# Performance work log

Measured on AMD Instinct MI355X. Metric: run time of the kernel, lower is better.

Reference implementation:

```python
import jax, jax.numpy as jnp
import numpy as np

B, CIN, T = 32, 64, 4096
E, H, HD, FF, L = 256, 8, 32, 1024, 4
K, S = 15, 2
SEQ = 512
GROUPS = E // 2
EPS = 1e-5


def setup_inputs() -> dict:
    key = jax.random.key(0)
    ks = jax.random.split(key, 16)
    d = {}
    d['x'] = jax.random.normal(ks[0], (B, CIN, T), jnp.float32)
    d['conv0_w'] = jax.random.normal(ks[1], (E, CIN, K), jnp.float32) * 0.03
    d['conv0_b'] = jnp.zeros((E,), jnp.float32)
    d['conv12_w'] = jax.random.normal(ks[2], (2, E, E, K), jnp.float32) * 0.016
    d['conv12_b'] = jnp.zeros((2, E), jnp.float32)
    d['gn_g'] = jnp.ones((3, E), jnp.float32)
    d['gn_b'] = jnp.zeros((3, E), jnp.float32)
    d['Wq'] = jax.random.normal(ks[3], (L, H, HD, E), jnp.float32) * 0.0625
    d['Wk'] = jax.random.normal(ks[4], (L, H, HD, E), jnp.float32) * 0.0625
    d['Wv'] = jax.random.normal(ks[5], (L, H, HD, E), jnp.float32) * 0.0625
    d['Wo'] = jax.random.normal(ks[6], (L, E, E), jnp.float32) * 0.0625
    d['ln1_g'] = jnp.ones((L, E), jnp.float32)
    d['ln1_b'] = jnp.zeros((L, E), jnp.float32)
    d['Wf1'] = jax.random.normal(ks[7], (L, FF, E), jnp.float32) * 0.0625
    d['bf1'] = jnp.zeros((L, FF), jnp.float32)
    d['Wf2'] = jax.random.normal(ks[8], (L, E, FF), jnp.float32) * 0.03125
    d['bf2'] = jnp.zeros((L, E), jnp.float32)
    d['ln2_g'] = jnp.ones((L, E), jnp.float32)
    d['ln2_b'] = jnp.zeros((L, E), jnp.float32)
    d['Wc1'] = jax.random.normal(ks[9], (256, SEQ * E), jnp.float32) * 0.003
    d['bc1'] = jnp.zeros((256,), jnp.float32)
    d['Wc2'] = jax.random.normal(ks[10], (1, 256), jnp.float32) * 0.0625
    d['bc2'] = jnp.zeros((1,), jnp.float32)
    return d


def conv1d(x, w, b, stride, pad):
    y = jax.lax.conv_general_dilated(x, w, (stride,), [(pad, pad)],
                                     dimension_numbers=('NCH', 'OIH', 'NCH'))
    return y + b[None, :, None]


def group_norm(x, g, b):
    # x: [B, C, Len]; torch GroupNorm with C//2 groups
    Bn, C, Ln = x.shape
    xg = x.reshape(Bn, GROUPS, C // GROUPS, Ln)
    mu = xg.mean(axis=(2, 3), keepdims=True)
    var = ((xg - mu) ** 2).mean(axis=(2, 3), keepdims=True)
    xn = ((xg - mu) * jax.lax.rsqrt(var + EPS)).reshape(Bn, C, Ln)
    return xn * g[None, :, None] + b[None, :, None]


def layer_norm(x, g, b):
    mu = x.mean(-1, keepdims=True)
    var = ((x - mu) ** 2).mean(-1, keepdims=True)
    return (x - mu) * jax.lax.rsqrt(var + EPS) * g + b


def pos_encoding(seq, e):
    t = jnp.arange(seq, dtype=jnp.float32)[:, None]
    i = jnp.arange(e, dtype=jnp.float32)[None, :]
    ang = t / jnp.power(10000.0, i / e)  # note: i/e, matching the source
    return jnp.where(jnp.arange(e)[None, :] % 2 == 0, jnp.sin(ang), jnp.cos(ang))


def reference(x, conv0_w, conv0_b, conv12_w, conv12_b, gn_g, gn_b,
              Wq, Wk, Wv, Wo, ln1_g, ln1_b, Wf1, bf1, Wf2, bf2,
              ln2_g, ln2_b, Wc1, bc1, Wc2, bc2):
    # --- conv encoder: (conv -> dropout(eval) -> groupnorm -> gelu) x3 ---
    h = conv1d(x, conv0_w, conv0_b, S, K // 2)
    h = jax.nn.gelu(group_norm(h, gn_g[0], gn_b[0]), approximate=False)
    for i in range(2):
        h = conv1d(h, conv12_w[i], conv12_b[i], S, K // 2)
        h = jax.nn.gelu(group_norm(h, gn_g[i + 1], gn_b[i + 1]), approximate=False)
    h = jnp.transpose(h, (0, 2, 1))  # [B, SEQ, E]

    # --- transformer encoder ---
    h = h + pos_encoding(h.shape[1], E)[None]
    scale = 1.0 / jnp.sqrt(jnp.float32(HD))
    for l in range(L):
        q = jnp.einsum('bse,hde->bhsd', h, Wq[l])
        k = jnp.einsum('bse,hde->bhsd', h, Wk[l])
        v = jnp.einsum('bse,hde->bhsd', h, Wv[l])
        attn = jax.nn.softmax(jnp.einsum('bhqd,bhkd->bhqk', q, k) * scale, axis=-1)
        o = jnp.einsum('bhqk,bhkd->bhqd', attn, v)
        o = jnp.transpose(o, (0, 2, 1, 3)).reshape(h.shape[0], h.shape[1], E)
        o = o @ Wo[l].T
        h1 = layer_norm(o + h, ln1_g[l], ln1_b[l])
        f = jax.nn.relu(h1 @ Wf1[l].T + bf1[l]) @ Wf2[l].T + bf2[l]
        h = layer_norm(f + h1, ln2_g[l], ln2_b[l])

    # --- binary classifier ---
    flat = h.reshape(h.shape[0], -1)  # [B, SEQ*E]
    hid = jax.nn.relu(flat @ Wc1.T + bc1)
    return jax.nn.sigmoid(hid @ Wc2.T + bc2)  # [B, 1]
```

## Files before the change

### kernel.cpp

```cpp
#include <hip/hip_runtime.h>
#include <math.h>


typedef unsigned int   u32;
typedef unsigned short u16;
typedef __attribute__((ext_vector_type(4))) float f32x4;
typedef __attribute__((ext_vector_type(8))) short bf16x8;

__device__ __forceinline__ u16 f2bf(float v) {
    union { float f; u32 u; } x; x.f = v;
    u32 r = x.u + 0x7fffu + ((x.u >> 16) & 1u);
    return (u16)(r >> 16);
}

__device__ __forceinline__ void gl2lds16(const void* gsrc, void* ldst) {
    __builtin_amdgcn_global_load_lds(
        (const __attribute__((address_space(1))) void*)gsrc,
        (__attribute__((address_space(3))) void*)ldst, 16, 0, 0);
}

__device__ __forceinline__ float maeeg_block_sum(float v, float* sc4) {
#pragma unroll
    for (int off = 32; off; off >>= 1) v += __shfl_down(v, off);
    int t = threadIdx.x;
    if ((t & 63) == 0) sc4[t >> 6] = v;
    __syncthreads();
    float r = sc4[0] + sc4[1] + sc4[2] + sc4[3];
    __syncthreads();
    return r;
}

__global__ __launch_bounds__(256) void maeeg_mm_kernel(
    const u16* __restrict__ Ag, const u16* __restrict__ Bg,
    const float* __restrict__ bias, const float* __restrict__ res,
    void* __restrict__ outp, int N, int K, int flags)
{
    __shared__ u16 As[8192];
    __shared__ u16 Bs[8192];
    const int m0 = blockIdx.x * 128, n0 = blockIdx.y * 128;
    const int t = threadIdx.x, w = t >> 6, lane = t & 63;
    const int fr = lane & 15, fq = lane >> 4;
    const int wm = (w >> 1) * 64, wn = (w & 1) * 64;
    const int srow = lane >> 3;
    const int srcc = (lane & 7) ^ srow;

    f32x4 acc[4][4];
    const f32x4 zero = {0.f, 0.f, 0.f, 0.f};
#pragma unroll
    for (int i = 0; i < 4; ++i)
#pragma unroll
        for (int j = 0; j < 4; ++j) acc[i][j] = zero;

    for (int k0 = 0; k0 < K; k0 += 64) {
#pragma unroll
        for (int j = 0; j < 4; ++j) {
            int rowb = w * 32 + j * 8;
            int r = rowb + srow;
            gl2lds16(Ag + (size_t)(m0 + r) * K + k0 + srcc * 8,
                     (char*)As + rowb * 128);
            gl2lds16(Bg + (size_t)(n0 + r) * K + k0 + srcc * 8,
                     (char*)Bs + rowb * 128);
        }
        __syncthreads();
#pragma unroll
        for (int kc = 0; kc < 2; ++kc) {
            bf16x8 af[4], bfv[4];
#pragma unroll
            for (int i = 0; i < 4; ++i) {
                int am = wm + i * 16 + fr;
                int bn = wn + i * 16 + fr;
                int kb = kc * 64 + fq * 16;
                af[i]  = *(const bf16x8*)((const char*)As + am * 128 + (kb ^ ((am & 7) << 4)));
                bfv[i] = *(const bf16x8*)((const char*)Bs + bn * 128 + (kb ^ ((bn & 7) << 4)));
            }
#pragma unroll
            for (int i = 0; i < 4; ++i)
#pragma unroll
                for (int j = 0; j < 4; ++j)
                    acc[i][j] = __builtin_amdgcn_mfma_f32_16x16x32_bf16(
                        af[i], bfv[j], acc[i][j], 0, 0, 0);
        }
        __syncthreads();
    }
#pragma unroll
    for (int i = 0; i < 4; ++i) {
#pragma unroll
        for (int j = 0; j < 4; ++j) {
            int n = n0 + wn + j * 16 + fr;
            float bv = bias ? bias[n] : 0.f;
#pragma unroll
            for (int r = 0; r < 4; ++r) {
                int m = m0 + wm + i * 16 + fq * 4 + r;
                float v = acc[i][j][r] + bv;
                if (res) v += res[(size_t)m * N + n];
                if (flags & 1) v = fmaxf(v, 0.f);
                if (flags & 16) {
                    u16* o = (u16*)outp;
                    int seg = n >> 8, nn = n & 255;
                    if (seg == 0)
                        o[(size_t)m * 256 + nn] = f2bf(v * 0.17677669529663687f);
                    else if (seg == 1)
                        o[4194304 + (size_t)m * 256 + nn] = f2bf(v);
                    else
                        o[8388608 + (((size_t)(m >> 9)) * 256 + nn) * 512 + (m & 511)] = f2bf(v);
                } else if (flags & 4)
                    ((u16*)outp)[(((size_t)(m >> 9)) * 256 + n) * 512 + (m & 511)] = f2bf(v);
                else if (flags & 2)
                    ((u16*)outp)[(size_t)m * N + n] = f2bf(v);
                else
                    ((float*)outp)[(size_t)m * N + n] = v;
            }
        }
    }
}

__global__ __launch_bounds__(512) void maeeg_mmln_kernel(
    const u16* __restrict__ Ag, const u16* __restrict__ Bg,
    const float* __restrict__ bias, const float* __restrict__ res,
    const float* __restrict__ g, const float* __restrict__ b,
    float* __restrict__ outf, u16* __restrict__ outb, int K)
{
    __shared__ u16 As[64 * 64];
    __shared__ u16 Bs[256 * 64];
    __shared__ float psum[64][4];
    __shared__ float psq[64][4];
    const int m0 = blockIdx.x * 64;
    const int t = threadIdx.x, w = t >> 6, lane = t & 63;
    const int fr = lane & 15, fq = lane >> 4;
    const int wm = (w & 1) * 32, wn = (w >> 1) * 64;
    const int seg = w >> 1;
    const int srow = lane >> 3;
    const int srcc = (lane & 7) ^ srow;

    f32x4 acc[2][4];
    const f32x4 zero = {0.f, 0.f, 0.f, 0.f};
#pragma unroll
    for (int i = 0; i < 2; ++i)
#pragma unroll
        for (int j = 0; j < 4; ++j) acc[i][j] = zero;

    for (int k0 = 0; k0 < K; k0 += 64) {
        gl2lds16(Ag + (size_t)(m0 + w * 8 + srow) * K + k0 + srcc * 8,
                 (char*)As + (w * 8) * 128);
#pragma unroll
        for (int j = 0; j < 4; ++j) {
            int rowb = w * 32 + j * 8;
            gl2lds16(Bg + (size_t)(rowb + srow) * K + k0 + srcc * 8,
                     (char*)Bs + rowb * 128);
        }
        __syncthreads();
#pragma unroll
        for (int kc = 0; kc < 2; ++kc) {
            int kb = kc * 64 + fq * 16;
            bf16x8 af[2], bfv[4];
#pragma unroll
            for (int i = 0; i < 2; ++i) {
                int am = wm + i * 16 + fr;
                af[i] = *(const bf16x8*)((const char*)As + am * 128 + (kb ^ ((am & 7) << 4)));
            }
#pragma unroll
            for (int j = 0; j < 4; ++j) {
                int bn = wn + j * 16 + fr;
                bfv[j] = *(const bf16x8*)((const char*)Bs + bn * 128 + (kb ^ ((bn & 7) << 4)));
            }
#pragma unroll
            for (int i = 0; i < 2; ++i)
#pragma unroll
                for (int j = 0; j < 4; ++j)
                    acc[i][j] = __builtin_amdgcn_mfma_f32_16x16x32_bf16(
                        af[i], bfv[j], acc[i][j], 0, 0, 0);
        }
        __syncthreads();
    }

#pragma unroll
    for (int j = 0; j < 4; ++j) {
        int n = wn + j * 16 + fr;
        float bv = bias ? bias[n] : 0.f;
#pragma unroll
        for (int i = 0; i < 2; ++i)
#pragma unroll
            for (int r = 0; r < 4; ++r) {
                int m = m0 + wm + i * 16 + fq * 4 + r;
                acc[i][j][r] += bv + res[(size_t)m * 256 + n];
            }
    }
#pragma unroll
    for (int i = 0; i < 2; ++i)
#pragma unroll
        for (int r = 0; r < 4; ++r) {
            float s = acc[i][0][r] + acc[i][1][r] + acc[i][2][r] + acc[i][3][r];
            float q = acc[i][0][r] * acc[i][0][r] + acc[i][1][r] * acc[i][1][r]
                    + acc[i][2][r] * acc[i][2][r] + acc[i][3][r] * acc[i][3][r];
#pragma unroll
            for (int off = 1; off < 16; off <<= 1) {
                s += __shfl_xor(s, off);
                q += __shfl_xor(q, off);
            }
            if (fr == 0) {
                int ml = wm + i * 16 + fq * 4 + r;
                psum[ml][seg] = s;
                psq[ml][seg] = q;
            }
        }
    __syncthreads();
#pragma unroll
    for (int i = 0; i < 2; ++i)
#pragma unroll
        for (int r = 0; r < 4; ++r) {
            int ml = wm + i * 16 + fq * 4 + r;
            float S = psum[ml][0] + psum[ml][1] + psum[ml][2] + psum[ml][3];
            float Q = psq[ml][0] + psq[ml][1] + psq[ml][2] + psq[ml][3];
            float mu = S * (1.f / 256.f);
            float var = fmaxf(Q * (1.f / 256.f) - mu * mu, 0.f);
            float rs = rsqrtf(var + 1e-5f);
            size_t mrow = (size_t)(m0 + ml) * 256;
#pragma unroll
            for (int j = 0; j < 4; ++j) {
                int n = wn + j * 16 + fr;
                float o = (acc[i][j][r] - mu) * rs * g[n] + b[n];
                if (outf) outf[mrow + n] = o;
                outb[mrow + n] = f2bf(o);
            }
        }
}

__global__ __launch_bounds__(256) void maeeg_convmm_kernel(
    const u16* __restrict__ Wp, const u16* __restrict__ inp,
    const float* __restrict__ cb, float* __restrict__ out,
    int K3, int len_in, int len_out)
{
    __shared__ u16 As[8192];
    __shared__ u16 Bs[8192];
    const int m0 = blockIdx.x * 128, t0 = blockIdx.y * 128, b = blockIdx.z;
    const int lip = len_in + 16;
    const u16* inb = inp + (size_t)b * (K3 >> 4) * lip;
    const int t = threadIdx.x, w = t >> 6, lane = t & 63;
    const int sr = lane & 7, sc = lane >> 3;
    const int fr = lane & 15, fq = lane >> 4;
    const int wm = (w >> 1) * 64, wn = (w & 1) * 64;
    const int srow = lane >> 3;
    const int srcc = (lane & 7) ^ srow;

    f32x4 acc[4][4];
    const f32x4 zero = {0.f, 0.f, 0.f, 0.f};
#pragma unroll
    for (int i = 0; i < 4; ++i)
#pragma unroll
        for (int j = 0; j < 4; ++j) acc[i][j] = zero;

    for (int k0 = 0; k0 < K3; k0 += 64) {
#pragma unroll
        for (int j = 0; j < 4; ++j) {
            int rowb = w * 32 + j * 8;
            gl2lds16(Wp + (size_t)(m0 + rowb + srow) * K3 + k0 + srcc * 8,
                     (char*)As + rowb * 128);
            int row = rowb + sr;
            int k  = k0 + sc * 8;
            int ci = k >> 4, rr = k & 15;
            int tg = t0 + row;
            const u16* gp = inb + (size_t)ci * lip + 2 * tg + rr;
            uint4 vb;
            vb.x = *(const u32*)(gp);
            vb.y = *(const u32*)(gp + 2);
            vb.z = *(const u32*)(gp + 4);
            vb.w = *(const u32*)(gp + 6);
            int kb = (sc ^ (row & 7)) << 4;
            *(uint4*)((char*)Bs + row * 128 + kb) = vb;
        }
        __syncthreads();
#pragma unroll
        for (int kc = 0; kc < 2; ++kc) {
            bf16x8 af[4], bfv[4];
#pragma unroll
            for (int i = 0; i < 4; ++i) {
                int am = wm + i * 16 + fr;
                int bn = wn + i * 16 + fr;
                int kb = kc * 64 + fq * 16;
                af[i]  = *(const bf16x8*)((const char*)As + am * 128 + (kb ^ ((am & 7) << 4)));
                bfv[i] = *(const bf16x8*)((const char*)Bs + bn * 128 + (kb ^ ((bn & 7) << 4)));
            }
#pragma unroll
            for (int i = 0; i < 4; ++i)
#pragma unroll
                for (int j = 0; j < 4; ++j)
                    acc[i][j] = __builtin_amdgcn_mfma_f32_16x16x32_bf16(
                        af[i], bfv[j], acc[i][j], 0, 0, 0);
        }
        __syncthreads();
    }
#pragma unroll
    for (int i = 0; i < 4; ++i) {
#pragma unroll
        for (int r = 0; r < 4; ++r) {
            int m = m0 + wm + i * 16 + fq * 4 + r;
            float bb = cb[m];
            float* op = out + ((size_t)b * 256 + m) * len_out + t0;
#pragma unroll
            for (int j = 0; j < 4; ++j)
                op[wn + j * 16 + fr] = acc[i][j][r] + bb;
        }
    }
}

__global__ __launch_bounds__(256) void maeeg_fattn_kernel(
    const u16* __restrict__ Qb, const u16* __restrict__ Kb,
    const u16* __restrict__ Vt, u16* __restrict__ att)
{
    __shared__ u16 Ks[64 * 32];
    __shared__ u16 Vs[32 * 64];
    __shared__ u16 Ps[4][32 * 64];
    const int qt = blockIdx.x, h = blockIdx.y, b = blockIdx.z;
    const int t = threadIdx.x, w = t >> 6, lane = t & 63;
    const int fr = lane & 15, fq = lane >> 4;
    const u16* qbase = Qb + (size_t)b * 512 * 256 + h * 32;
    const u16* kbase = Kb + (size_t)b * 512 * 256 + h * 32;
    const u16* vbase = Vt + (size_t)b * 256 * 512 + (size_t)h * 32 * 512;

    bf16x8 qf[2];
#pragma unroll
    for (int mi = 0; mi < 2; ++mi)
        qf[mi] = *(const bf16x8*)(qbase +
                 (size_t)(qt * 128 + w * 32 + mi * 16 + fr) * 256 + fq * 8);

    f32x4 oacc[2][2];
    const f32x4 zero = {0.f, 0.f, 0.f, 0.f};
    oacc[0][0] = zero; oacc[0][1] = zero; oacc[1][0] = zero; oacc[1][1] = zero;
    float mrun[8], lrun[8];
#pragma unroll
    for (int i = 0; i < 8; ++i) { mrun[i] = -1e30f; lrun[i] = 0.f; }

    for (int kt = 0; kt < 512; kt += 64) {
        {
            int row = t >> 2, c = t & 3;
            uint4 kv = *(const uint4*)(kbase + (size_t)(kt + row) * 256 + c * 8);
            *(uint4*)((char*)Ks + row * 64 + (((c ^ (row & 3)) << 4))) = kv;
            int d = t >> 3, c2 = t & 7;
            uint4 vv = *(const uint4*)(vbase + (size_t)d * 512 + kt + c2 * 8);
            *(uint4*)((char*)Vs + d * 128 + ((c2 ^ (d & 7)) << 4)) = vv;
        }
        __syncthreads();

        f32x4 sacc[2][4];
#pragma unroll
        for (int mi = 0; mi < 2; ++mi)
#pragma unroll
            for (int ni = 0; ni < 4; ++ni) sacc[mi][ni] = zero;
        bf16x8 kf[4];
#pragma unroll
        for (int ni = 0; ni < 4; ++ni) {
            int kk = ni * 16 + fr;
            kf[ni] = *(const bf16x8*)((const char*)Ks + kk * 64 +
                                      ((fq ^ (kk & 3)) << 4));
        }
#pragma unroll
        for (int mi = 0; mi < 2; ++mi)
#pragma unroll
            for (int ni = 0; ni < 4; ++ni)
                sacc[mi][ni] = __builtin_amdgcn_mfma_f32_16x16x32_bf16(
                    qf[mi], kf[ni], sacc[mi][ni], 0, 0, 0);

#pragma unroll
        for (int mi = 0; mi < 2; ++mi) {
#pragma unroll
            for (int reg = 0; reg < 4; ++reg) {
                int idx = mi * 4 + reg;
                float rm = fmaxf(fmaxf(sacc[mi][0][reg], sacc[mi][1][reg]),
                                 fmaxf(sacc[mi][2][reg], sacc[mi][3][reg]));
                rm = fmaxf(rm, __shfl_xor(rm, 1));
                rm = fmaxf(rm, __shfl_xor(rm, 2));
                rm = fmaxf(rm, __shfl_xor(rm, 4));
                rm = fmaxf(rm, __shfl_xor(rm, 8));
                float mold = mrun[idx];
                float mnew = fmaxf(mold, rm);
                float c = __expf(mold - mnew);
                mrun[idx] = mnew;
                int q = mi * 16 + fq * 4 + reg;
                float psum = 0.f;
#pragma unroll
                for (int ni = 0; ni < 4; ++ni) {
                    float p = __expf(sacc[mi][ni][reg] - mnew);
                    psum += p;
                    int kk = ni * 16 + fr;
                    int boff = q * 128 + ((((kk >> 3) ^ (q & 7)) << 4) | ((kk & 7) << 1));
                    *(u16*)((char*)Ps[w] + boff) = f2bf(p);
                }
                lrun[idx] = lrun[idx] * c + psum;
                oacc[mi][0][reg] *= c;
                oacc[mi][1][reg] *= c;
            }
        }

        bf16x8 pf[2][2], vf[2][2];
#pragma unroll
        for (int mi = 0; mi < 2; ++mi)
#pragma unroll
            for (int kc = 0; kc < 2; ++kc) {
                int q = mi * 16 + fr;
                int ch = (kc * 4 + fq) ^ (q & 7);
                pf[mi][kc] = *(const bf16x8*)((const char*)Ps[w] + q * 128 + (ch << 4));
            }
#pragma unroll
        for (int nj = 0; nj < 2; ++nj)
#pragma unroll
            for (int kc = 0; kc < 2; ++kc) {
                int d = nj * 16 + fr;
                int ch = (kc * 4 + fq) ^ (d & 7);
                vf[nj][kc] = *(const bf16x8*)((const char*)Vs + d * 128 + (ch << 4));
            }
#pragma unroll
        for (int mi = 0; mi < 2; ++mi)
#pragma unroll
            for (int nj = 0; nj < 2; ++nj) {
                oacc[mi][nj] = __builtin_amdgcn_mfma_f32_16x16x32_bf16(
                    pf[mi][0], vf[nj][0], oacc[mi][nj], 0, 0, 0);
                oacc[mi][nj] = __builtin_amdgcn_mfma_f32_16x16x32_bf16(
                    pf[mi][1], vf[nj][1], oacc[mi][nj], 0, 0, 0);
            }
        __syncthreads();
    }

#pragma unroll
    for (int idx = 0; idx < 8; ++idx) {
        float l = lrun[idx];
        l += __shfl_xor(l, 1);
        l += __shfl_xor(l, 2);
        l += __shfl_xor(l, 4);
        l += __shfl_xor(l, 8);
        lrun[idx] = 1.f / l;
    }
    u16* ob = att + (size_t)b * 512 * 256 + h * 32;
#pragma unroll
    for (int mi = 0; mi < 2; ++mi)
#pragma unroll
        for (int reg = 0; reg < 4; ++reg) {
            int q = qt * 128 + w * 32 + mi * 16 + fq * 4 + reg;
            float inv = lrun[mi * 4 + reg];
#pragma unroll
            for (int nj = 0; nj < 2; ++nj)
                ob[(size_t)q * 256 + nj * 16 + fr] =
                    f2bf(oacc[mi][nj][reg] * inv);
        }
}

__global__ void maeeg_prep_convw_kernel(const float* __restrict__ src,
                                        u16* __restrict__ dst, int nrows)
{
    int i = blockIdx.x * 256 + threadIdx.x;
    if (i >= nrows) return;
    const float* s = src + (size_t)i * 15;
    float4 a = *(const float4*)s;
    float4 b = *(const float4*)(s + 4);
    float4 c = *(const float4*)(s + 8);
    float e12 = s[12], e13 = s[13], e14 = s[14];
    uint4 p0, p1;
    p0.x = (u32)f2bf(a.x) | ((u32)f2bf(a.y) << 16);
    p0.y = (u32)f2bf(a.z) | ((u32)f2bf(a.w) << 16);
    p0.z = (u32)f2bf(b.x) | ((u32)f2bf(b.y) << 16);
    p0.w = (u32)f2bf(b.z) | ((u32)f2bf(b.w) << 16);
    p1.x = (u32)f2bf(c.x) | ((u32)f2bf(c.y) << 16);
    p1.y = (u32)f2bf(c.z) | ((u32)f2bf(c.w) << 16);
    p1.z = (u32)f2bf(e12) | ((u32)f2bf(e13) << 16);
    p1.w = (u32)f2bf(e14);
    uint4* d = (uint4*)(dst + (size_t)i * 16);
    d[0] = p0; d[1] = p1;
}

__device__ __forceinline__ uint4 pack8(const float* s) {
    float4 a = ((const float4*)s)[0];
    float4 b = ((const float4*)s)[1];
    uint4 p;
    p.x = (u32)f2bf(a.x) | ((u32)f2bf(a.y) << 16);
    p.y = (u32)f2bf(a.z) | ((u32)f2bf(a.w) << 16);
    p.z = (u32)f2bf(b.x) | ((u32)f2bf(b.y) << 16);
    p.w = (u32)f2bf(b.z) | ((u32)f2bf(b.w) << 16);
    return p;
}

__global__ void maeeg_cast_www_kernel(
    const float* __restrict__ Wo, u16* __restrict__ dWo,
    const float* __restrict__ Wf1, u16* __restrict__ dWf1,
    const float* __restrict__ Wf2, u16* __restrict__ dWf2)
{
    int i = blockIdx.x * 256 + threadIdx.x;
    const float* s; u16* d; int off;
    if (i < 32768)       { s = Wo;  d = dWo;  off = i; }
    else if (i < 163840) { s = Wf1; d = dWf1; off = i - 32768; }
    else                 { s = Wf2; d = dWf2; off = i - 163840; }
    *(uint4*)(d + (size_t)off * 8) = pack8(s + (size_t)off * 8);
}

__global__ void maeeg_cast_qkv3_kernel(
    const float* __restrict__ Wq, const float* __restrict__ Wk,
    const float* __restrict__ Wv, u16* __restrict__ dst)
{
    int seg = blockIdx.y;
    const float* src = (seg == 0) ? Wq : ((seg == 1) ? Wk : Wv);
    int i = blockIdx.x * 256 + threadIdx.x;
    int l = i >> 13, r = (i & 8191) * 8;
    *(uint4*)(dst + (size_t)l * 196608 + seg * 65536 + r) =
        pack8(src + (size_t)i * 8);
}

__global__ void maeeg_cast_pad_kernel(const float* __restrict__ src,
                                      u16* __restrict__ dst, int len)
{
    int lip = len + 16;
    int n8 = lip >> 3;
    int i = blockIdx.x * 256 + threadIdx.x;
    if (i >= n8) return;
    int row = blockIdx.y;
    int p0 = i * 8;
    u16 vals[8];
#pragma unroll
    for (int e = 0; e < 8; ++e) {
        int q = p0 + e - 7;
        vals[e] = (q >= 0 && q < len) ? f2bf(src[(size_t)row * len + q]) : (u16)0;
    }
    uint4 pk;
    pk.x = (u32)vals[0] | ((u32)vals[1] << 16);
    pk.y = (u32)vals[2] | ((u32)vals[3] << 16);
    pk.z = (u32)vals[4] | ((u32)vals[5] << 16);
    pk.w = (u32)vals[6] | ((u32)vals[7] << 16);
    *(uint4*)(dst + (size_t)row * lip + p0) = pk;
}

__global__ void maeeg_pe_kernel(float* __restrict__ pet)
{
    int s = blockIdx.x, e = threadIdx.x;
    float ang = (float)s / powf(10000.f, (float)e * (1.f / 256.f));
    pet[s * 256 + e] = (e & 1) ? cosf(ang) : sinf(ang);
}

__global__ __launch_bounds__(256) void maeeg_gn_gelu_kernel(
    float* __restrict__ h, const float* __restrict__ g,
    const float* __restrict__ bta, int len, u16* __restrict__ bfout, int lip,
    int keep32)
{
    const int grp = blockIdx.x, b = blockIdx.y;
    float* p = h + ((size_t)b * 256 + grp * 2) * len;
    const int n = 2 * len;
    float s1 = 0.f, s2 = 0.f;
    for (int i = threadIdx.x; i < n; i += 256) {
        float v = p[i];
        s1 += v; s2 += v * v;
    }
    __shared__ float sc[4];
    float S1 = maeeg_block_sum(s1, sc);
    float S2 = maeeg_block_sum(s2, sc);
    float mu = S1 / (float)n;
    float var = fmaxf(S2 / (float)n - mu * mu, 0.f);
    float rs = rsqrtf(var + 1e-5f);
    float g0 = g[grp * 2], g1 = g[grp * 2 + 1];
    float b0 = bta[grp * 2], b1 = bta[grp * 2 + 1];
    u16* bp = bfout ? bfout + ((size_t)b * 256 + grp * 2) * lip : (u16*)0;
    for (int i = threadIdx.x; i < n; i += 256) {
        float v = (p[i] - mu) * rs;
        float y = (i < len) ? (v * g0 + b0) : (v * g1 + b1);
        float ge = 0.5f * y * (1.f + erff(y * 0.70710678118654752f));
        if (keep32) p[i] = ge;
        if (bp) bp[(i < len ? i : (i - len) + lip) + 7] = f2bf(ge);
    }
    if (bp && threadIdx.x < 32) {
        int ch = threadIdx.x >> 4, pp = threadIdx.x & 15;
        bp[(size_t)ch * lip + ((pp < 7) ? pp : (len + pp))] = 0;
    }
}

__global__ __launch_bounds__(256) void maeeg_transpose_pos_kernel(
    const float* __restrict__ in, const float* __restrict__ pet,
    float* __restrict__ out, u16* __restrict__ outb)
{
    __shared__ float tile[256][33];
    const int s0 = blockIdx.x * 32, b = blockIdx.y;
    for (int idx = threadIdx.x; idx < 256 * 32; idx += 256) {
        int e = idx >> 5, j = idx & 31;
        tile[e][j] = in[((size_t)b * 256 + e) * 512 + s0 + j];
    }
    __syncthreads();
    for (int idx = threadIdx.x; idx < 32 * 256; idx += 256) {
        int j = idx >> 8, e = idx & 255;
        float v = tile[e][j] + pet[(s0 + j) * 256 + e];
        size_t o = ((size_t)b * 512 + s0 + j) * 256 + e;
        out[o] = v;
        outb[o] = f2bf(v);
    }
}

__global__ __launch_bounds__(256) void maeeg_cls1_kernel(
    const u16* __restrict__ flatb, const float* __restrict__ Wc1,
    float* __restrict__ part)
{
    __shared__ u16 As[32 * 64];
    __shared__ u16 Bs[64 * 64];
    const int ks = blockIdx.x, jt = blockIdx.y;
    const int t = threadIdx.x, w = t >> 6, lane = t & 63;
    const int fr = lane & 15, fq = lane >> 4;
    const int kbase0 = ks * 1024;
    const int brow = t >> 2, bq = t & 3;
    const int srow = lane >> 3;
    const int srcc = (lane & 7) ^ srow;

    f32x4 acc[2];
    const f32x4 zero = {0.f, 0.f, 0.f, 0.f};
    acc[0] = zero; acc[1] = zero;

    for (int step = 0; step < 16; ++step) {
        int kk = kbase0 + step * 64;
        int rowb = w * 8;
        gl2lds16(flatb + (size_t)(rowb + srow) * 131072 + kk + srcc * 8,
                 (char*)As + rowb * 128);
        const float* wp = Wc1 + (size_t)(jt * 64 + brow) * 131072 + kk + bq * 16;
        float4 f0 = ((const float4*)wp)[0];
        float4 f1 = ((const float4*)wp)[1];
        float4 f2 = ((const float4*)wp)[2];
        float4 f3 = ((const float4*)wp)[3];
        uint4 p0, p1;
        p0.x = (u32)f2bf(f0.x) | ((u32)f2bf(f0.y) << 16);
        p0.y = (u32)f2bf(f0.z) | ((u32)f2bf(f0.w) << 16);
        p0.z = (u32)f2bf(f1.x) | ((u32)f2bf(f1.y) << 16);
        p0.w = (u32)f2bf(f1.z) | ((u32)f2bf(f1.w) << 16);
        p1.x = (u32)f2bf(f2.x) | ((u32)f2bf(f2.y) << 16);
        p1.y = (u32)f2bf(f2.z) | ((u32)f2bf(f2.w) << 16);
        p1.z = (u32)f2bf(f3.x) | ((u32)f2bf(f3.y) << 16);
        p1.w = (u32)f2bf(f3.z) | ((u32)f2bf(f3.w) << 16);
        int c0 = bq * 2, c1 = bq * 2 + 1;
        *(uint4*)((char*)Bs + brow * 128 + ((c0 ^ (brow & 7)) << 4)) = p0;
        *(uint4*)((char*)Bs + brow * 128 + ((c1 ^ (brow & 7)) << 4)) = p1;
        __syncthreads();
#pragma unroll
        for (int kc = 0; kc < 2; ++kc) {
            int kbyte = kc * 64 + fq * 16;
            int bn = w * 16 + fr;
            bf16x8 bfv = *(const bf16x8*)((const char*)Bs + bn * 128 +
                                          (kbyte ^ ((bn & 7) << 4)));
#pragma unroll
            for (int mi = 0; mi < 2; ++mi) {
                int am = mi * 16 + fr;
                bf16x8 af = *(const bf16x8*)((const char*)As + am * 128 +
                                             (kbyte ^ ((am & 7) << 4)));
                acc[mi] = __builtin_amdgcn_mfma_f32_16x16x32_bf16(
                    af, bfv, acc[mi], 0, 0, 0);
            }
        }
        __syncthreads();
    }
#pragma unroll
    for (int mi = 0; mi < 2; ++mi)
#pragma unroll
        for (int r = 0; r < 4; ++r) {
            int m = mi * 16 + fq * 4 + r;
            int j = jt * 64 + w * 16 + fr;
            part[((size_t)ks * 32 + m) * 256 + j] = acc[mi][r];
        }
}

__global__ __launch_bounds__(256) void maeeg_cls23_kernel(
    const float* __restrict__ part, const float* __restrict__ bc1,
    const float* __restrict__ Wc2, const float* __restrict__ bc2,
    float* __restrict__ out)
{
    const int b = blockIdx.x, j = threadIdx.x;
    float s = bc1[j];
    for (int ks = 0; ks < 128; ++ks) s += part[((size_t)ks * 32 + b) * 256 + j];
    float v = fmaxf(s, 0.f) * Wc2[j];
    __shared__ float sc[4];
    float tot = maeeg_block_sum(v, sc);
    if (j == 0) out[b] = 1.f / (1.f + expf(-(tot + bc2[0])));
}

extern "C" void kernel_launch(void* const* d_in, const int* in_sizes, int n_in,
                              void* d_out, int out_size, void* d_ws, size_t ws_size,
                              hipStream_t stream)
{
    (void)in_sizes; (void)n_in; (void)out_size; (void)ws_size;
    const float* x        = (const float*)d_in[0];
    const float* conv0_w  = (const float*)d_in[1];
    const float* conv0_b  = (const float*)d_in[2];
    const float* conv12_w = (const float*)d_in[3];
    const float* conv12_b = (const float*)d_in[4];
    const float* gn_g     = (const float*)d_in[5];
    const float* gn_b     = (const float*)d_in[6];
    const float* Wq       = (const float*)d_in[7];
    const float* Wk       = (const float*)d_in[8];
    const float* Wv       = (const float*)d_in[9];
    const float* Wo       = (const float*)d_in[10];
    const float* ln1_g    = (const float*)d_in[11];
    const float* ln1_b    = (const float*)d_in[12];
    const float* Wf1      = (const float*)d_in[13];
    const float* bf1      = (const float*)d_in[14];
    const float* Wf2      = (const float*)d_in[15];
    const float* bf2      = (const float*)d_in[16];
    const float* ln2_g    = (const float*)d_in[17];
    const float* ln2_b    = (const float*)d_in[18];
    const float* Wc1      = (const float*)d_in[19];
    const float* bc1      = (const float*)d_in[20];
    const float* Wc2      = (const float*)d_in[21];
    const float* bc2      = (const float*)d_in[22];
    float* out = (float*)d_out;

    char* wsb = (char*)d_ws;
    u16* WB0   = (u16*)(wsb + 0);
    u16* WB12  = (u16*)(wsb + 524288);
    u16* WQKVb = (u16*)(wsb + 4718592);
    u16* WOb   = (u16*)(wsb + 6291456);
    u16* WF1b  = (u16*)(wsb + 6815744);
    u16* WF2b  = (u16*)(wsb + 8912896);
    u16*   XPAD  = (u16*)(wsb + 11010048);
    u16*   GN1B  = (u16*)(wsb + 11010048);
    float* D     = (float*)(wsb + 11010048);
    float* CONV0 = (float*)(wsb + 28049408);
    float* CONV1 = (float*)(wsb + 28049408);
    float* CONV2 = (float*)(wsb + 28049408 + 33554432);
    u16*   Qb2   = (u16*)(wsb + 28049408);
    u16*   ATTb  = (u16*)(wsb + 28049408 + 25165824);
    u16*   Db    = (u16*)(wsb + 28049408 + 33554432);
    u16*   F1b   = (u16*)(wsb + 28049408);
    u16*   GN0B  = (u16*)(wsb + 95158272);
    float* C     = (float*)(wsb + 95158272);
    u16*   Cb    = (u16*)(wsb + 95158272 + 16777216);
    float* PART  = (float*)(wsb + 128974848);
    float* PET   = (float*)(wsb + 133201920);

    maeeg_prep_convw_kernel<<<64, 256, 0, stream>>>(conv0_w, WB0, 16384);
    maeeg_prep_convw_kernel<<<512, 256, 0, stream>>>(conv12_w, WB12, 131072);
    maeeg_cast_qkv3_kernel<<<dim3(128, 3), 256, 0, stream>>>(Wq, Wk, Wv, WQKVb);
    maeeg_cast_www_kernel<<<1152, 256, 0, stream>>>(Wo, WOb, Wf1, WF1b, Wf2, WF2b);
    maeeg_cast_pad_kernel<<<dim3(3, 2048), 256, 0, stream>>>(x, XPAD, 4096);
    maeeg_pe_kernel<<<512, 256, 0, stream>>>(PET);

    maeeg_convmm_kernel<<<dim3(2, 16, 32), 256, 0, stream>>>(
        WB0, XPAD, conv0_b, CONV0, 1024, 4096, 2048);
    maeeg_gn_gelu_kernel<<<dim3(128, 32), 256, 0, stream>>>(
        CONV0, gn_g, gn_b, 2048, GN0B, 2064, 0);
    maeeg_convmm_kernel<<<dim3(2, 8, 32), 256, 0, stream>>>(
        WB12, GN0B, conv12_b, CONV1, 4096, 2048, 1024);
    maeeg_gn_gelu_kernel<<<dim3(128, 32), 256, 0, stream>>>(
        CONV1, gn_g + 256, gn_b + 256, 1024, GN1B, 1040, 0);
    maeeg_convmm_kernel<<<dim3(2, 4, 32), 256, 0, stream>>>(
        WB12 + 256 * 4096, GN1B, conv12_b + 256, CONV2, 4096, 1024, 512);
    maeeg_gn_gelu_kernel<<<dim3(128, 32), 256, 0, stream>>>(
        CONV2, gn_g + 512, gn_b + 512, 512, (u16*)0, 0, 1);
    maeeg_transpose_pos_kernel<<<dim3(16, 32), 256, 0, stream>>>(CONV2, PET, C, Cb);

    for (int l = 0; l < 4; ++l) {
        maeeg_mm_kernel<<<dim3(128, 6), 256, 0, stream>>>(
            Cb, WQKVb + l * 196608, (const float*)0, (const float*)0,
            Qb2, 256, 256, 16);
        maeeg_fattn_kernel<<<dim3(4, 8, 32), 256, 0, stream>>>(
            Qb2, Qb2 + 4194304, Qb2 + 8388608, ATTb);
        maeeg_mmln_kernel<<<256, 512, 0, stream>>>(
            ATTb, WOb + l * 65536, (const float*)0, C,
            ln1_g + l * 256, ln1_b + l * 256, D, Db, 256);
        maeeg_mm_kernel<<<dim3(128, 8), 256, 0, stream>>>(
            Db, WF1b + l * 262144, bf1 + l * 1024, (const float*)0, F1b, 1024, 256, 3);
        maeeg_mmln_kernel<<<256, 512, 0, stream>>>(
            F1b, WF2b + l * 262144, bf2 + l * 256, D,
            ln2_g + l * 256, ln2_b + l * 256, (l == 3) ? (float*)0 : C, Cb, 1024);
    }

    maeeg_cls1_kernel<<<dim3(128, 4), 256, 0, stream>>>(Cb, Wc1, PART);
    maeeg_cls23_kernel<<<32, 256, 0, stream>>>(PART, bc1, Wc2, bc2, out);
}
```

Baseline: 941.4 us.

## Store conv outputs as bf16, double-buffer attention K/V with async LDS loads

Conv GEMM outputs are now written in bf16 instead of fp32, and the GroupNorm+GELU kernel reads the packed bf16 pairs, with the last stage writing fp32 to a separate buffer. This halves the memory traffic between the conv and normalization stages. The flash attention kernel double-buffers K/V tiles using global_load_lds prefetch, hoists the V fragment loads, and packs P stores into 8-byte writes via lane shuffles. The trade-off is that the conv activations lose precision before the GroupNorm statistics are computed.

```diff
diff --git a/kernel.cpp b/kernel.cpp
--- a/kernel.cpp
+++ b/kernel.cpp
@@ -227,7 +227,7 @@
 
 __global__ __launch_bounds__(256) void maeeg_convmm_kernel(
     const u16* __restrict__ Wp, const u16* __restrict__ inp,
-    const float* __restrict__ cb, float* __restrict__ out,
+    const float* __restrict__ cb, u16* __restrict__ out,
     int K3, int len_in, int len_out)
 {
     __shared__ u16 As[8192];
@@ -295,10 +295,10 @@
         for (int r = 0; r < 4; ++r) {
             int m = m0 + wm + i * 16 + fq * 4 + r;
             float bb = cb[m];
-            float* op = out + ((size_t)b * 256 + m) * len_out + t0;
+            u16* op = out + ((size_t)b * 256 + m) * len_out + t0;
 #pragma unroll
             for (int j = 0; j < 4; ++j)
-                op[wn + j * 16 + fr] = acc[i][j][r] + bb;
+                op[wn + j * 16 + fr] = f2bf(acc[i][j][r] + bb);
         }
     }
 }
@@ -307,8 +307,8 @@
     const u16* __restrict__ Qb, const u16* __restrict__ Kb,
     const u16* __restrict__ Vt, u16* __restrict__ att)
 {
-    __shared__ u16 Ks[64 * 32];
-    __shared__ u16 Vs[32 * 64];
+    __shared__ u16 Ks[2][64 * 32];
+    __shared__ u16 Vs[2][32 * 64];
     __shared__ u16 Ps[4][32 * 64];
     const int qt = blockIdx.x, h = blockIdx.y, b = blockIdx.z;
     const int t = threadIdx.x, w = t >> 6, lane = t & 63;
@@ -317,6 +317,11 @@
     const u16* kbase = Kb + (size_t)b * 512 * 256 + h * 32;
     const u16* vbase = Vt + (size_t)b * 256 * 512 + (size_t)h * 32 * 512;
 
+    const int krow = w * 16 + (lane >> 2);
+    const int kcc  = (lane & 3) ^ (krow & 3);
+    const int vd   = w * 8 + (lane >> 3);
+    const int vcc  = (lane & 7) ^ (vd & 7);
+
     bf16x8 qf[2];
 #pragma unroll
     for (int mi = 0; mi < 2; ++mi)
@@ -330,16 +335,19 @@
 #pragma unroll
     for (int i = 0; i < 8; ++i) { mrun[i] = -1e30f; lrun[i] = 0.f; }
 
-    for (int kt = 0; kt < 512; kt += 64) {
-        {
-            int row = t >> 2, c = t & 3;
-            uint4 kv = *(const uint4*)(kbase + (size_t)(kt + row) * 256 + c * 8);
-            *(uint4*)((char*)Ks + row * 64 + (((c ^ (row & 3)) << 4))) = kv;
-            int d = t >> 3, c2 = t & 7;
-            uint4 vv = *(const uint4*)(vbase + (size_t)d * 512 + kt + c2 * 8);
-            *(uint4*)((char*)Vs + d * 128 + ((c2 ^ (d & 7)) << 4)) = vv;
-        }
-        __syncthreads();
+    gl2lds16(kbase + (size_t)krow * 256 + kcc * 8, (char*)Ks[0] + w * 1024);
+    gl2lds16(vbase + (size_t)vd * 512 + vcc * 8, (char*)Vs[0] + w * 1024);
+    __syncthreads();
+
+    int buf = 0;
+    for (int ti = 0; ti < 8; ++ti) {
+        if (ti < 7) {
+            int ktn = (ti + 1) * 64;
+            gl2lds16(kbase + (size_t)(ktn + krow) * 256 + kcc * 8,
+                     (char*)Ks[buf ^ 1] + w * 1024);
+            gl2lds16(vbase + (size_t)vd * 512 + ktn + vcc * 8,
+                     (char*)Vs[buf ^ 1] + w * 1024);
+        }
 
         f32x4 sacc[2][4];
 #pragma unroll
@@ -350,9 +358,18 @@
 #pragma unroll
         for (int ni = 0; ni < 4; ++ni) {
             int kk = ni * 16 + fr;
-            kf[ni] = *(const bf16x8*)((const char*)Ks + kk * 64 +
+            kf[ni] = *(const bf16x8*)((const char*)Ks[buf] + kk * 64 +
                                       ((fq ^ (kk & 3)) << 4));
         }
+        bf16x8 vf[2][2];
+#pragma unroll
+        for (int nj = 0; nj < 2; ++nj)
+#pragma unroll
+            for (int kc = 0; kc < 2; ++kc) {
+                int d = nj * 16 + fr;
+                int ch = (kc * 4 + fq) ^ (d & 7);
+                vf[nj][kc] = *(const bf16x8*)((const char*)Vs[buf] + d * 128 + (ch << 4));
+            }
 #pragma unroll
         for (int mi = 0; mi < 2; ++mi)
 #pragma unroll
@@ -376,22 +393,35 @@
                 float c = __expf(mold - mnew);
                 mrun[idx] = mnew;
                 int q = mi * 16 + fq * 4 + reg;
+                float pv[4];
                 float psum = 0.f;
 #pragma unroll
                 for (int ni = 0; ni < 4; ++ni) {
-                    float p = __expf(sacc[mi][ni][reg] - mnew);
-                    psum += p;
-                    int kk = ni * 16 + fr;
-                    int boff = q * 128 + ((((kk >> 3) ^ (q & 7)) << 4) | ((kk & 7) << 1));
-                    *(u16*)((char*)Ps[w] + boff) = f2bf(p);
+                    pv[ni] = __expf(sacc[mi][ni][reg] - mnew);
+                    psum += pv[ni];
                 }
+                float tq[4], uq[4], wq[4];
+#pragma unroll
+                for (int i = 0; i < 4; ++i) tq[i] = __shfl_xor(pv[i ^ 1], 1);
+#pragma unroll
+                for (int i = 0; i < 4; ++i) uq[i] = ((fr ^ i) & 1) ? tq[i] : pv[i];
+#pragma unroll
+                for (int i = 0; i < 4; ++i) tq[i] = __shfl_xor(uq[i ^ 2], 2);
+#pragma unroll
+                for (int i = 0; i < 4; ++i) wq[i] = ((fr ^ i) & 2) ? tq[i] : uq[i];
+                int col0 = (fr & 3) * 16 + (fr & 12);
+                int boff = q * 128 + ((((col0 >> 3) ^ (q & 7)) << 4) | ((col0 & 7) << 1));
+                uint2 pk;
+                pk.x = (u32)f2bf(wq[0]) | ((u32)f2bf(wq[1]) << 16);
+                pk.y = (u32)f2bf(wq[2]) | ((u32)f2bf(wq[3]) << 16);
+                *(uint2*)((char*)Ps[w] + boff) = pk;
                 lrun[idx] = lrun[idx] * c + psum;
                 oacc[mi][0][reg] *= c;
                 oacc[mi][1][reg] *= c;
             }
         }
 
-        bf16x8 pf[2][2], vf[2][2];
+        bf16x8 pf[2][2];
 #pragma unroll
         for (int mi = 0; mi < 2; ++mi)
 #pragma unroll
@@ -399,14 +429,6 @@
                 int q = mi * 16 + fr;
                 int ch = (kc * 4 + fq) ^ (q & 7);
                 pf[mi][kc] = *(const bf16x8*)((const char*)Ps[w] + q * 128 + (ch << 4));
-            }
-#pragma unroll
-        for (int nj = 0; nj < 2; ++nj)
-#pragma unroll
-            for (int kc = 0; kc < 2; ++kc) {
-                int d = nj * 16 + fr;
-                int ch = (kc * 4 + fq) ^ (d & 7);
-                vf[nj][kc] = *(const bf16x8*)((const char*)Vs + d * 128 + (ch << 4));
             }
 #pragma unroll
         for (int mi = 0; mi < 2; ++mi)
@@ -418,6 +440,7 @@
                     pf[mi][1], vf[nj][1], oacc[mi][nj], 0, 0, 0);
             }
         __syncthreads();
+        buf ^= 1;
     }
 
 #pragma unroll
@@ -533,33 +556,52 @@
 }
 
 __global__ __launch_bounds__(256) void maeeg_gn_gelu_kernel(
-    float* __restrict__ h, const float* __restrict__ g,
+    const u16* __restrict__ hin, const float* __restrict__ g,
     const float* __restrict__ bta, int len, u16* __restrict__ bfout, int lip,
-    int keep32)
+    float* __restrict__ f32out)
 {
     const int grp = blockIdx.x, b = blockIdx.y;
-    float* p = h + ((size_t)b * 256 + grp * 2) * len;
-    const int n = 2 * len;
+    const size_t base = ((size_t)b * 256 + grp * 2) * len;
+    const u32* p32 = (const u32*)(hin + base);
     float s1 = 0.f, s2 = 0.f;
-    for (int i = threadIdx.x; i < n; i += 256) {
-        float v = p[i];
-        s1 += v; s2 += v * v;
+    for (int i = threadIdx.x; i < len; i += 256) {
+        u32 v = p32[i];
+        union { u32 u; float f; } lo, hi;
+        lo.u = v << 16; hi.u = v & 0xffff0000u;
+        s1 += lo.f + hi.f;
+        s2 += lo.f * lo.f + hi.f * hi.f;
     }
     __shared__ float sc[4];
     float S1 = maeeg_block_sum(s1, sc);
     float S2 = maeeg_block_sum(s2, sc);
-    float mu = S1 / (float)n;
-    float var = fmaxf(S2 / (float)n - mu * mu, 0.f);
+    const float nn = (float)(2 * len);
+    float mu = S1 / nn;
+    float var = fmaxf(S2 / nn - mu * mu, 0.f);
     float rs = rsqrtf(var + 1e-5f);
     float g0 = g[grp * 2], g1 = g[grp * 2 + 1];
     float b0 = bta[grp * 2], b1 = bta[grp * 2 + 1];
     u16* bp = bfout ? bfout + ((size_t)b * 256 + grp * 2) * lip : (u16*)0;
-    for (int i = threadIdx.x; i < n; i += 256) {
-        float v = (p[i] - mu) * rs;
-        float y = (i < len) ? (v * g0 + b0) : (v * g1 + b1);
-        float ge = 0.5f * y * (1.f + erff(y * 0.70710678118654752f));
-        if (keep32) p[i] = ge;
-        if (bp) bp[(i < len ? i : (i - len) + lip) + 7] = f2bf(ge);
+    float* fp = f32out ? f32out + base : (float*)0;
+    for (int i2 = threadIdx.x; i2 < len; i2 += 256) {
+        u32 v = p32[i2];
+        int i = i2 * 2;
+        union { u32 u; float f; } lo, hi;
+        lo.u = v << 16; hi.u = v & 0xffff0000u;
+        bool c1 = (i >= len);
+        float gg = c1 ? g1 : g0, bb = c1 ? b1 : b0;
+        float y0 = (lo.f - mu) * rs * gg + bb;
+        float y1 = (hi.f - mu) * rs * gg + bb;
+        float e0 = 0.5f * y0 * (1.f + erff(y0 * 0.70710678118654752f));
+        float e1 = 0.5f * y1 * (1.f + erff(y1 * 0.70710678118654752f));
+        if (bp) {
+            int j0 = (i < len ? i : i - len + lip) + 7;
+            bp[j0] = f2bf(e0);
+            bp[j0 + 1] = f2bf(e1);
+        }
+        if (fp) {
+            fp[i] = e0;
+            fp[i + 1] = e1;
+        }
     }
     if (bp && threadIdx.x < 32) {
         int ch = threadIdx.x >> 4, pp = threadIdx.x & 15;
@@ -709,9 +751,10 @@
     u16*   XPAD  = (u16*)(wsb + 11010048);
     u16*   GN1B  = (u16*)(wsb + 11010048);
     float* D     = (float*)(wsb + 11010048);
-    float* CONV0 = (float*)(wsb + 28049408);
-    float* CONV1 = (float*)(wsb + 28049408);
-    float* CONV2 = (float*)(wsb + 28049408 + 33554432);
+    u16*   CONV0B = (u16*)(wsb + 28049408);
+    u16*   CONV1B = (u16*)(wsb + 28049408);
+    u16*   CONV2B = (u16*)(wsb + 28049408 + 33554432);
+    float* GN2F   = (float*)(wsb + 28049408);
     u16*   Qb2   = (u16*)(wsb + 28049408);
     u16*   ATTb  = (u16*)(wsb + 28049408 + 25165824);
     u16*   Db    = (u16*)(wsb + 28049408 + 33554432);
@@ -730,18 +773,18 @@
     maeeg_pe_kernel<<<512, 256, 0, stream>>>(PET);
 
     maeeg_convmm_kernel<<<dim3(2, 16, 32), 256, 0, stream>>>(
-        WB0, XPAD, conv0_b, CONV0, 1024, 4096, 2048);
+        WB0, XPAD, conv0_b, CONV0B, 1024, 4096, 2048);
     maeeg_gn_gelu_kernel<<<dim3(128, 32), 256, 0, stream>>>(
-        CONV0, gn_g, gn_b, 2048, GN0B, 2064, 0);
+        CONV0B, gn_g, gn_b, 2048, GN0B, 2064, (float*)0);
     maeeg_convmm_kernel<<<dim3(2, 8, 32), 256, 0, stream>>>(
-        WB12, GN0B, conv12_b, CONV1, 4096, 2048, 1024);
+        WB12, GN0B, conv12_b, CONV1B, 4096, 2048, 1024);
     maeeg_gn_gelu_kernel<<<dim3(128, 32), 256, 0, stream>>>(
-        CONV1, gn_g + 256, gn_b + 256, 1024, GN1B, 1040, 0);
+        CONV1B, gn_g + 256, gn_b + 256, 1024, GN1B, 1040, (float*)0);
     maeeg_convmm_kernel<<<dim3(2, 4, 32), 256, 0, stream>>>(
-        WB12 + 256 * 4096, GN1B, conv12_b + 256, CONV2, 4096, 1024, 512);
+        WB12 + 256 * 4096, GN1B, conv12_b + 256, CONV2B, 4096, 1024, 512);
     maeeg_gn_gelu_kernel<<<dim3(128, 32), 256, 0, stream>>>(
-        CONV2, gn_g + 512, gn_b + 512, 512, (u16*)0, 0, 1);
-    maeeg_transpose_pos_kernel<<<dim3(16, 32), 256, 0, stream>>>(CONV2, PET, C, Cb);
+        CONV2B, gn_g + 512, gn_b + 512, 512, (u16*)0, 0, GN2F);
+    maeeg_transpose_pos_kernel<<<dim3(16, 32), 256, 0, stream>>>(GN2F, PET, C, Cb);
 
     for (int l = 0; l < 4; ++l) {
         maeeg_mm_kernel<<<dim3(128, 6), 256, 0, stream>>>(
```

After: 967.8 us. +2.8%, slower.
